# Optimization experiments

Hardware: AMD Instinct MI355X
Metric: run time of the kernel (lower is better)

Reference implementation:

```python
import jax, jax.numpy as jnp
import numpy as np

B, P, N, C, H, E, HORIZON = 4, 8, 10000, 64, 256, 160000, 4


def setup_inputs() -> dict:
    key = jax.random.key(0)
    ks = jax.random.split(key, 32)
    rn = lambda k, shape, s=0.05: jax.random.normal(k, shape, jnp.float32) * s
    inp = {
        "x_seq": rn(ks[0], (B, P, N, C), 1.0),
        "ei0": jax.random.randint(ks[1], (2, E), 0, N, dtype=jnp.int32),
        "ei1": jax.random.randint(ks[2], (2, E), 0, N, dtype=jnp.int32),
        "Wl0": rn(ks[3], (C, H)), "bl0": jnp.zeros((H,), jnp.float32), "Wr0": rn(ks[4], (C, H)),
        "Wl1": rn(ks[5], (C, H)), "bl1": jnp.zeros((H,), jnp.float32), "Wr1": rn(ks[6], (C, H)),
        "Wp": rn(ks[7], (C, H)), "bp": jnp.zeros((C,), jnp.float32),
    }
    i = 8
    for g in ("g1", "g2", "g3"):
        inp[g + "_Wih"] = rn(ks[i], (3 * H, H)); i += 1
        inp[g + "_Whh"] = rn(ks[i], (3 * H, H)); i += 1
        inp[g + "_bih"] = jnp.zeros((3 * H,), jnp.float32)
        inp[g + "_bhh"] = jnp.zeros((3 * H,), jnp.float32)
    return inp


def _sage(x, src, dst, Wl, bl, Wr, n_nodes):
    # PyG SAGEConv (mean aggr): lin_l(mean_j x_j) + lin_r(x_i); lin_r has no bias.
    agg = jax.ops.segment_sum(x[src], dst, num_segments=n_nodes)  # [n, C]
    cnt = jax.ops.segment_sum(jnp.ones((src.shape[0],), x.dtype), dst, num_segments=n_nodes)
    agg = agg / jnp.maximum(cnt, 1.0)[:, None]
    return agg @ Wl + bl + x @ Wr


def _gru(x, h, Wih, Whh, bih, bhh):
    gi = x @ Wih.T + bih
    gh = h @ Whh.T + bhh
    ir, iz, inn = jnp.split(gi, 3, axis=1)
    hr, hz, hn = jnp.split(gh, 3, axis=1)
    r = jax.nn.sigmoid(ir + hr)
    z = jax.nn.sigmoid(iz + hz)
    n = jnp.tanh(inn + r * hn)
    return (1.0 - z) * n + z * h


def reference(x_seq, ei0, ei1,
              Wl0, bl0, Wr0, Wl1, bl1, Wr1,
              g1_Wih, g1_Whh, g1_bih, g1_bhh,
              g2_Wih, g2_Whh, g2_bih, g2_bhh,
              g3_Wih, g3_Whh, g3_bih, g3_bhh,
              Wp, bp):
    Bn = B * N
    off = (jnp.arange(B) * N).astype(ei0.dtype)
    batch = lambda ei: (ei[:, None, :] + off[None, :, None]).reshape(2, -1)
    b0, b1 = batch(ei0), batch(ei1)

    def step(xt, h1, h2, h3):
        c = (_sage(xt, b0[0], b0[1], Wl0, bl0, Wr0, Bn)
             + _sage(xt, b1[0], b1[1], Wl1, bl1, Wr1, Bn))  # HeteroConv aggr='sum'
        c = jax.nn.relu(c)  # dropout is identity in eval
        h1 = _gru(c, h1, g1_Wih, g1_Whh, g1_bih, g1_bhh)
        h2 = _gru(h1, h2, g2_Wih, g2_Whh, g2_bih, g2_bhh)
        h3 = _gru(h2, h3, g3_Wih, g3_Whh, g3_bih, g3_bhh)
        return h1, h2, h3

    h0 = jnp.zeros((Bn, H), x_seq.dtype)
    xs = jnp.transpose(x_seq, (1, 0, 2, 3)).reshape(P, Bn, C)

    def enc_body(carry, xt):
        return step(xt, *carry), None

    (h1, h2, h3), _ = jax.lax.scan(enc_body, (h0, h0, h0), xs)

    def dec_body(carry, _):
        h1, h2, h3, xd = carry
        h1, h2, h3 = step(xd, h1, h2, h3)
        y = h3 @ Wp.T + bp  # [Bn, C]
        return (h1, h2, h3, y), y

    x_dec = x_seq[:, -1].reshape(Bn, C)
    _, ys = jax.lax.scan(dec_body, (h1, h2, h3, x_dec), None, length=HORIZON)
    # ys: [HORIZON, Bn, C] -> [B, HORIZON, N, C]
    return jnp.transpose(ys.reshape(HORIZON, B, N, C), (1, 0, 2, 3))
```

## Files before the change

kernel.cpp:

```cpp
#include <hip/hip_runtime.h>
#include <hip/hip_bf16.h>
#include <cstdint>

#define B_   4
#define P_   8
#define N_   10000
#define C_   64
#define H_   256
#define E_   160000
#define HOR_ 4
#define BN_  (B_ * N_)
#define MPAD 40064

typedef __bf16 bf16;
typedef __attribute__((ext_vector_type(8))) __bf16 bf16x8;
typedef __attribute__((ext_vector_type(4))) float f32x4;

__device__ __forceinline__ void gl2lds16(const bf16* g, bf16* l) {
    __builtin_amdgcn_global_load_lds(
        (const __attribute__((address_space(1))) void*)g,
        (__attribute__((address_space(3))) void*)l, 16, 0, 0);
}

template <int BIAS, int RELU, int OUTBF, int PROJ>
__global__ __launch_bounds__(256) void gemm_k(
    const bf16* __restrict__ A, const bf16* __restrict__ Bt,
    void* __restrict__ Cp, const float* __restrict__ bias,
    int K, int Nn, int tstep)
{
    __shared__ __align__(16) bf16 As[128 * 32];
    __shared__ __align__(16) bf16 Bs[128 * 32];

    const int tid  = threadIdx.x;
    const int m0   = blockIdx.y * 128;
    const int n0   = blockIdx.x * 128;
    const int wave = tid >> 6;
    const int lane = tid & 63;
    const int wm   = (wave >> 1) << 6;
    const int wn   = (wave & 1) << 6;
    const int lr   = lane & 15;
    const int kg   = lane >> 4;

    f32x4 acc[4][4] = {};

    const int r0 = tid >> 2;
    const int k0 = (tid & 3) << 3;

    for (int kk = 0; kk < K; kk += 32) {
        const bf16* ga = A  + (size_t)(m0 + r0) * K + kk + k0;
        const bf16* gb = Bt + (size_t)(n0 + r0) * K + kk + k0;
        gl2lds16(ga,                  As + tid * 8);
        gl2lds16(ga + 64 * (size_t)K, As + 2048 + tid * 8);
        gl2lds16(gb,                  Bs + tid * 8);
        gl2lds16(gb + 64 * (size_t)K, Bs + 2048 + tid * 8);
        __syncthreads();

        bf16x8 af[4], bfv[4];
#pragma unroll
        for (int i = 0; i < 4; ++i)
            af[i] = *reinterpret_cast<const bf16x8*>(&As[(wm + i * 16 + lr) * 32 + kg * 8]);
#pragma unroll
        for (int j = 0; j < 4; ++j)
            bfv[j] = *reinterpret_cast<const bf16x8*>(&Bs[(wn + j * 16 + lr) * 32 + kg * 8]);
#pragma unroll
        for (int i = 0; i < 4; ++i)
#pragma unroll
            for (int j = 0; j < 4; ++j)
                acc[i][j] = __builtin_amdgcn_mfma_f32_16x16x32_bf16(af[i], bfv[j], acc[i][j], 0, 0, 0);
        __syncthreads();
    }

#pragma unroll
    for (int i = 0; i < 4; ++i) {
#pragma unroll
        for (int j = 0; j < 4; ++j) {
#pragma unroll
            for (int v = 0; v < 4; ++v) {
                int row = m0 + wm + i * 16 + kg * 4 + v;
                int col = n0 + wn + j * 16 + lr;
                float val = acc[i][j][v];
                if (BIAS) val += bias[col];
                if (RELU) val = fmaxf(val, 0.f);
                if (PROJ) {
                    if (col < C_ && row < BN_) {
                        int b = row / N_, n = row - b * N_;
                        reinterpret_cast<float*>(Cp)[(((size_t)b * HOR_ + tstep) * N_ + n) * C_ + col] = val;
                    }
                } else if (OUTBF) {
                    reinterpret_cast<bf16*>(Cp)[(size_t)row * Nn + col] = (bf16)val;
                } else {
                    reinterpret_cast<float*>(Cp)[(size_t)row * Nn + col] = val;
                }
            }
        }
    }
}

__global__ __launch_bounds__(256, 2) void gru_fused_k(
    const bf16* __restrict__ X, const bf16* __restrict__ Hc,
    bf16* __restrict__ Hn,
    const bf16* __restrict__ Wih, const bf16* __restrict__ Whh,
    const float* __restrict__ bih, const float* __restrict__ bhh)
{
    const int id    = blockIdx.x;
    const int sblk  = id >> 6;
    const int jblk  = (id >> 3) & 7;
    const int slow  = id & 7;
    const int strip = (sblk << 3) | slow;
    if (strip >= 313) return;

    __shared__ __align__(16) bf16 Xs[128 * 32];
    __shared__ __align__(16) bf16 Hs[128 * 32];
    __shared__ __align__(16) bf16 Ws[6 * 32 * 32];

    const int tid  = threadIdx.x;
    const int m0   = strip * 128;
    const int j0   = jblk * 32;
    const int wave = tid >> 6;
    const int lane = tid & 63;
    const int wm   = (wave >> 1) << 6;
    const int wn   = (wave & 1) << 4;
    const int lr   = lane & 15;
    const int kg   = lane >> 4;

    f32x4 acc[6][4] = {};

    const int r0 = tid >> 2;
    const int k0 = (tid & 3) << 3;

    int wgate[3], wrow[3], wk[3];
#pragma unroll
    for (int c = 0; c < 3; ++c) {
        int f = c * 2048 + tid * 8;
        wgate[c] = f >> 10;
        wrow[c]  = (f >> 5) & 31;
        wk[c]    = f & 31;
    }

    for (int kk = 0; kk < 256; kk += 32) {
        gl2lds16(X  + (size_t)(m0 + r0) * 256 + kk + k0,      Xs + tid * 8);
        gl2lds16(X  + (size_t)(m0 + r0 + 64) * 256 + kk + k0, Xs + 2048 + tid * 8);
        gl2lds16(Hc + (size_t)(m0 + r0) * 256 + kk + k0,      Hs + tid * 8);
        gl2lds16(Hc + (size_t)(m0 + r0 + 64) * 256 + kk + k0, Hs + 2048 + tid * 8);
#pragma unroll
        for (int c = 0; c < 3; ++c) {
            int g = wgate[c];
            const bf16* src = (g < 3)
                ? Wih + (size_t)(g * 256 + j0 + wrow[c]) * 256 + kk + wk[c]
                : Whh + (size_t)((g - 3) * 256 + j0 + wrow[c]) * 256 + kk + wk[c];
            gl2lds16(src, Ws + c * 2048 + tid * 8);
        }
        __syncthreads();

        bf16x8 af[4], ah[4], bw[6];
#pragma unroll
        for (int i = 0; i < 4; ++i) {
            af[i] = *reinterpret_cast<const bf16x8*>(&Xs[(wm + i * 16 + lr) * 32 + kg * 8]);
            ah[i] = *reinterpret_cast<const bf16x8*>(&Hs[(wm + i * 16 + lr) * 32 + kg * 8]);
        }
#pragma unroll
        for (int g = 0; g < 6; ++g)
            bw[g] = *reinterpret_cast<const bf16x8*>(&Ws[g * 1024 + (wn + lr) * 32 + kg * 8]);
#pragma unroll
        for (int g = 0; g < 3; ++g)
#pragma unroll
            for (int i = 0; i < 4; ++i)
                acc[g][i] = __builtin_amdgcn_mfma_f32_16x16x32_bf16(af[i], bw[g], acc[g][i], 0, 0, 0);
#pragma unroll
        for (int g = 3; g < 6; ++g)
#pragma unroll
            for (int i = 0; i < 4; ++i)
                acc[g][i] = __builtin_amdgcn_mfma_f32_16x16x32_bf16(ah[i], bw[g], acc[g][i], 0, 0, 0);
        __syncthreads();
    }

    const int col = j0 + wn + lr;
    const float bi_r = bih[col], bi_z = bih[256 + col], bi_n = bih[512 + col];
    const float bh_r = bhh[col], bh_z = bhh[256 + col], bh_n = bhh[512 + col];
#pragma unroll
    for (int i = 0; i < 4; ++i) {
#pragma unroll
        for (int v = 0; v < 4; ++v) {
            int row = m0 + wm + i * 16 + kg * 4 + v;
            float ir  = acc[0][i][v] + bi_r;
            float iz  = acc[1][i][v] + bi_z;
            float in_ = acc[2][i][v] + bi_n;
            float hr  = acc[3][i][v] + bh_r;
            float hz  = acc[4][i][v] + bh_z;
            float hn  = acc[5][i][v] + bh_n;
            float r = __fdividef(1.f, 1.f + __expf(-(ir + hr)));
            float z = __fdividef(1.f, 1.f + __expf(-(iz + hz)));
            float a = in_ + r * hn;
            a = fminf(fmaxf(a, -15.f), 15.f);
            float t2 = __expf(2.f * a);
            float nn = __fdividef(t2 - 1.f, t2 + 1.f);
            float hold = (float)Hc[(size_t)row * 256 + col];
            Hn[(size_t)row * 256 + col] = (bf16)((1.f - z) * nn + z * hold);
        }
    }
}

struct __attribute__((aligned(8))) bf4 { bf16 b[4]; };

__global__ __launch_bounds__(256) void gather_conv_k(
    const float* __restrict__ xbase, long long sB, long long sN,
    const int* __restrict__ rp0, const int* __restrict__ col0,
    const int* __restrict__ rp1, const int* __restrict__ col1,
    bf16* __restrict__ Aconv)
{
    int wid  = (blockIdx.x * 256 + threadIdx.x) >> 6;
    int lane = threadIdx.x & 63;
    if (wid >= BN_) return;
    int b = wid / N_;
    int n = wid - b * N_;
    int eg = lane >> 4;
    int cl = lane & 15;
    const float* xb = xbase + (size_t)b * sB;

    float4 xv = *reinterpret_cast<const float4*>(&xb[(size_t)n * sN + cl * 4]);

    float4 s0 = {0.f, 0.f, 0.f, 0.f};
    int st = rp0[n], en = rp0[n + 1];
    float d0 = fmaxf((float)(en - st), 1.f);
    for (int e = st + eg; e < en; e += 4) {
        const float4 v = *reinterpret_cast<const float4*>(&xb[(size_t)col0[e] * sN + cl * 4]);
        s0.x += v.x; s0.y += v.y; s0.z += v.z; s0.w += v.w;
    }

    float4 s1 = {0.f, 0.f, 0.f, 0.f};
    st = rp1[n]; en = rp1[n + 1];
    float d1 = fmaxf((float)(en - st), 1.f);
    for (int e = st + eg; e < en; e += 4) {
        const float4 v = *reinterpret_cast<const float4*>(&xb[(size_t)col1[e] * sN + cl * 4]);
        s1.x += v.x; s1.y += v.y; s1.z += v.z; s1.w += v.w;
    }

#pragma unroll
    for (int m = 16; m <= 32; m <<= 1) {
        s0.x += __shfl_xor(s0.x, m, 64); s0.y += __shfl_xor(s0.y, m, 64);
        s0.z += __shfl_xor(s0.z, m, 64); s0.w += __shfl_xor(s0.w, m, 64);
        s1.x += __shfl_xor(s1.x, m, 64); s1.y += __shfl_xor(s1.y, m, 64);
        s1.z += __shfl_xor(s1.z, m, 64); s1.w += __shfl_xor(s1.w, m, 64);
    }

    if (eg == 0) {
        float r0 = 1.f / d0, r1 = 1.f / d1;
        bf16* row = Aconv + (size_t)wid * 192;
        bf4 o;
        o.b[0] = (bf16)(s0.x * r0); o.b[1] = (bf16)(s0.y * r0);
        o.b[2] = (bf16)(s0.z * r0); o.b[3] = (bf16)(s0.w * r0);
        *reinterpret_cast<bf4*>(&row[cl * 4]) = o;
        o.b[0] = (bf16)xv.x; o.b[1] = (bf16)xv.y; o.b[2] = (bf16)xv.z; o.b[3] = (bf16)xv.w;
        *reinterpret_cast<bf4*>(&row[64 + cl * 4]) = o;
        o.b[0] = (bf16)(s1.x * r1); o.b[1] = (bf16)(s1.y * r1);
        o.b[2] = (bf16)(s1.z * r1); o.b[3] = (bf16)(s1.w * r1);
        *reinterpret_cast<bf4*>(&row[128 + cl * 4]) = o;
    }
}

__global__ void count_k(const int* __restrict__ ei, int* __restrict__ cnt) {
    int e = blockIdx.x * 256 + threadIdx.x;
    if (e < E_) atomicAdd(&cnt[ei[E_ + e]], 1);
}

__global__ __launch_bounds__(1024) void scan_k(
    const int* __restrict__ cnt, int* __restrict__ rp, int* __restrict__ fill)
{
    __shared__ int sums[1024];
    int t = threadIdx.x;
    const int chunk = 10;
    int lo = t * chunk;
    int hi = lo + chunk; if (hi > N_) hi = N_;
    int s = 0;
    for (int i = lo; i < hi; ++i) s += cnt[i];
    sums[t] = s;
    __syncthreads();
    for (int off = 1; off < 1024; off <<= 1) {
        int u = (t >= off) ? sums[t - off] : 0;
        __syncthreads();
        sums[t] += u;
        __syncthreads();
    }
    int base = (t == 0) ? 0 : sums[t - 1];
    for (int i = lo; i < hi; ++i) { rp[i] = base; fill[i] = base; base += cnt[i]; }
    if (t == 1023) rp[N_] = sums[1023];
}

__global__ void fill_k(const int* __restrict__ ei, int* __restrict__ fill,
                       int* __restrict__ colarr) {
    int e = blockIdx.x * 256 + threadIdx.x;
    if (e < E_) {
        int p = atomicAdd(&fill[ei[E_ + e]], 1);
        colarr[p] = ei[e];
    }
}

__global__ void cvt_bf16_k(const float* __restrict__ s, bf16* __restrict__ d, int n) {
    int i = blockIdx.x * 256 + threadIdx.x;
    if (i < n) d[i] = (bf16)s[i];
}

__global__ void build_conv_bt_k(const float* __restrict__ Wl0, const float* __restrict__ Wr0,
                                const float* __restrict__ Wl1, const float* __restrict__ Wr1,
                                bf16* __restrict__ Bt) {
    int idx = blockIdx.x * 256 + threadIdx.x;
    if (idx >= 256 * 192) return;
    int n = idx / 192, k = idx - n * 192;
    float v;
    if (k < 64)       v = Wl0[k * 256 + n];
    else if (k < 128) v = Wr0[(k - 64) * 256 + n] + Wr1[(k - 64) * 256 + n];
    else              v = Wl1[(k - 128) * 256 + n];
    Bt[idx] = (bf16)v;
}

__global__ void build_conv_bias_k(const float* __restrict__ bl0, const float* __restrict__ bl1,
                                  float* __restrict__ bias) {
    int i = threadIdx.x;
    if (i < 256) bias[i] = bl0[i] + bl1[i];
}

__global__ void build_proj_k(const float* __restrict__ Wp, const float* __restrict__ bp,
                             bf16* __restrict__ Bt, float* __restrict__ bias) {
    int idx = blockIdx.x * 256 + threadIdx.x;
    if (idx < 128 * 256) {
        int n = idx >> 8, k = idx & 255;
        Bt[idx] = (bf16)(n < 64 ? Wp[n * 256 + k] : 0.f);
    }
    if (idx < 128) bias[idx] = (idx < 64) ? bp[idx] : 0.f;
}

extern "C" void kernel_launch(void* const* d_in, const int* in_sizes, int n_in,
                              void* d_out, int out_size, void* d_ws, size_t ws_size,
                              hipStream_t stream)
{
    const float* x_seq = (const float*)d_in[0];
    const int*   ei0   = (const int*)d_in[1];
    const int*   ei1   = (const int*)d_in[2];
    const float* Wl0   = (const float*)d_in[3];
    const float* bl0   = (const float*)d_in[4];
    const float* Wr0   = (const float*)d_in[5];
    const float* Wl1   = (const float*)d_in[6];
    const float* bl1   = (const float*)d_in[7];
    const float* Wr1   = (const float*)d_in[8];
    const float* Wp    = (const float*)d_in[9];
    const float* bp    = (const float*)d_in[10];
    const float* gWih[3], *gWhh[3], *gbih[3], *gbhh[3];
    for (int g = 0; g < 3; ++g) {
        gWih[g] = (const float*)d_in[11 + 4 * g];
        gWhh[g] = (const float*)d_in[12 + 4 * g];
        gbih[g] = (const float*)d_in[13 + 4 * g];
        gbhh[g] = (const float*)d_in[14 + 4 * g];
    }

    char* p = (char*)d_ws;
    auto alloc = [&](size_t bytes) -> char* {
        char* r = p; p += (bytes + 255) & ~(size_t)255; return r;
    };
    bf16*  Aconv  = (bf16*)alloc((size_t)MPAD * 192 * 2);
    bf16*  cbuf   = (bf16*)alloc((size_t)MPAD * 256 * 2);
    bf16*  hbuf[6];
    for (int g = 0; g < 6; ++g) hbuf[g] = (bf16*)alloc((size_t)MPAD * 256 * 2);
    bf16*  wih[3], *whh[3];
    for (int g = 0; g < 3; ++g) {
        wih[g] = (bf16*)alloc((size_t)768 * 256 * 2);
        whh[g] = (bf16*)alloc((size_t)768 * 256 * 2);
    }
    bf16*  btconv = (bf16*)alloc((size_t)256 * 192 * 2);
    float* bconv  = (float*)alloc(256 * 4);
    bf16*  btproj = (bf16*)alloc((size_t)128 * 256 * 2);
    float* bproj  = (float*)alloc(128 * 4);
    int* cnt0  = (int*)alloc(N_ * 4);
    int* cnt1  = (int*)alloc(N_ * 4);
    int* rp0   = (int*)alloc((N_ + 1) * 4);
    int* rp1   = (int*)alloc((N_ + 1) * 4);
    int* fill0 = (int*)alloc((N_ + 1) * 4);
    int* fill1 = (int*)alloc((N_ + 1) * 4);
    int* col0  = (int*)alloc(E_ * 4);
    int* col1  = (int*)alloc(E_ * 4);

    hipMemsetAsync(Aconv, 0, (size_t)MPAD * 192 * 2, stream);
    for (int g = 0; g < 3; ++g)
        hipMemsetAsync(hbuf[g], 0, (size_t)MPAD * 256 * 2, stream);
    hipMemsetAsync(cnt0, 0, N_ * 4, stream);
    hipMemsetAsync(cnt1, 0, N_ * 4, stream);

    for (int g = 0; g < 3; ++g) {
        cvt_bf16_k<<<768, 256, 0, stream>>>(gWih[g], wih[g], 768 * 256);
        cvt_bf16_k<<<768, 256, 0, stream>>>(gWhh[g], whh[g], 768 * 256);
    }
    build_conv_bt_k<<<192, 256, 0, stream>>>(Wl0, Wr0, Wl1, Wr1, btconv);
    build_conv_bias_k<<<1, 256, 0, stream>>>(bl0, bl1, bconv);
    build_proj_k<<<128, 256, 0, stream>>>(Wp, bp, btproj, bproj);

    count_k<<<(E_ + 255) / 256, 256, 0, stream>>>(ei0, cnt0);
    count_k<<<(E_ + 255) / 256, 256, 0, stream>>>(ei1, cnt1);
    scan_k<<<1, 1024, 0, stream>>>(cnt0, rp0, fill0);
    scan_k<<<1, 1024, 0, stream>>>(cnt1, rp1, fill1);
    fill_k<<<(E_ + 255) / 256, 256, 0, stream>>>(ei0, fill0, col0);
    fill_k<<<(E_ + 255) / 256, 256, 0, stream>>>(ei1, fill1, col1);

    bf16 *hc[3] = { hbuf[0], hbuf[1], hbuf[2] };
    bf16 *hn[3] = { hbuf[3], hbuf[4], hbuf[5] };

    auto do_conv = [&](const float* xb, long long sB, long long sN) {
        gather_conv_k<<<10000, 256, 0, stream>>>(xb, sB, sN, rp0, col0, rp1, col1, Aconv);
        gemm_k<1, 1, 1, 0><<<dim3(2, 313, 1), 256, 0, stream>>>(
            Aconv, btconv, cbuf, bconv, 192, 256, 0);
    };
    auto do_grus = [&]() {
        gru_fused_k<<<2560, 256, 0, stream>>>(
            cbuf, hc[0], hn[0], wih[0], whh[0], gbih[0], gbhh[0]);
        gru_fused_k<<<2560, 256, 0, stream>>>(
            hn[0], hc[1], hn[1], wih[1], whh[1], gbih[1], gbhh[1]);
        gru_fused_k<<<2560, 256, 0, stream>>>(
            hn[1], hc[2], hn[2], wih[2], whh[2], gbih[2], gbhh[2]);
        for (int g = 0; g < 3; ++g) { bf16* t = hc[g]; hc[g] = hn[g]; hn[g] = t; }
    };

    for (int ps = 0; ps < P_; ++ps) {
        do_conv(x_seq + (size_t)ps * N_ * C_, (long long)P_ * N_ * C_, C_);
        do_grus();
    }

    float* out = (float*)d_out;
    for (int t = 0; t < HOR_; ++t) {
        if (t > 0)
            do_conv(out + (size_t)(t - 1) * N_ * C_, (long long)HOR_ * N_ * C_, C_);
        do_grus();
        gemm_k<1, 0, 0, 1><<<dim3(1, 313, 1), 256, 0, stream>>>(
            hc[2], btproj, out, bproj, 256, 128, t);
    }
}
```

Before: 2.782 ms.

## Double-buffer LDS tiles in GEMM and fused GRU kernels to overlap loads

Both the generic GEMM kernel and the fused GRU kernel now keep two LDS buffers per operand. The next K-slice is issued via global_load_lds while MFMAs run on the current slice, and only one barrier is taken per iteration. The aim is to hide global memory latency behind compute. It doubles LDS use per block, which may reduce occupancy, most likely in the GRU kernel, which already declares launch bounds of 2 blocks per CU.

```diff
diff --git a/kernel.cpp b/kernel.cpp
--- a/kernel.cpp
+++ b/kernel.cpp
@@ -28,8 +28,8 @@
     void* __restrict__ Cp, const float* __restrict__ bias,
     int K, int Nn, int tstep)
 {
-    __shared__ __align__(16) bf16 As[128 * 32];
-    __shared__ __align__(16) bf16 Bs[128 * 32];
+    __shared__ __align__(16) bf16 As[2][128 * 32];
+    __shared__ __align__(16) bf16 Bs[2][128 * 32];
 
     const int tid  = threadIdx.x;
     const int m0   = blockIdx.y * 128;
@@ -46,29 +46,40 @@
     const int r0 = tid >> 2;
     const int k0 = (tid & 3) << 3;
 
-    for (int kk = 0; kk < K; kk += 32) {
+    auto stage = [&](int buf, int kk) {
         const bf16* ga = A  + (size_t)(m0 + r0) * K + kk + k0;
         const bf16* gb = Bt + (size_t)(n0 + r0) * K + kk + k0;
-        gl2lds16(ga,                  As + tid * 8);
-        gl2lds16(ga + 64 * (size_t)K, As + 2048 + tid * 8);
-        gl2lds16(gb,                  Bs + tid * 8);
-        gl2lds16(gb + 64 * (size_t)K, Bs + 2048 + tid * 8);
-        __syncthreads();
-
+        gl2lds16(ga,                  &As[buf][tid * 8]);
+        gl2lds16(ga + 64 * (size_t)K, &As[buf][2048 + tid * 8]);
+        gl2lds16(gb,                  &Bs[buf][tid * 8]);
+        gl2lds16(gb + 64 * (size_t)K, &Bs[buf][2048 + tid * 8]);
+    };
+
+    auto compute = [&](int cb) {
         bf16x8 af[4], bfv[4];
 #pragma unroll
         for (int i = 0; i < 4; ++i)
-            af[i] = *reinterpret_cast<const bf16x8*>(&As[(wm + i * 16 + lr) * 32 + kg * 8]);
+            af[i] = *reinterpret_cast<const bf16x8*>(&As[cb][(wm + i * 16 + lr) * 32 + kg * 8]);
 #pragma unroll
         for (int j = 0; j < 4; ++j)
-            bfv[j] = *reinterpret_cast<const bf16x8*>(&Bs[(wn + j * 16 + lr) * 32 + kg * 8]);
+            bfv[j] = *reinterpret_cast<const bf16x8*>(&Bs[cb][(wn + j * 16 + lr) * 32 + kg * 8]);
 #pragma unroll
         for (int i = 0; i < 4; ++i)
 #pragma unroll
             for (int j = 0; j < 4; ++j)
                 acc[i][j] = __builtin_amdgcn_mfma_f32_16x16x32_bf16(af[i], bfv[j], acc[i][j], 0, 0, 0);
+    };
+
+    stage(0, 0);
+    __syncthreads();
+    int cur = 0;
+    for (int kk = 32; kk < K; kk += 32) {
+        stage(cur ^ 1, kk);
+        compute(cur);
         __syncthreads();
-    }
+        cur ^= 1;
+    }
+    compute(cur);
 
 #pragma unroll
     for (int i = 0; i < 4; ++i) {
@@ -109,9 +120,9 @@
     const int strip = (sblk << 3) | slow;
     if (strip >= 313) return;
 
-    __shared__ __align__(16) bf16 Xs[128 * 32];
-    __shared__ __align__(16) bf16 Hs[128 * 32];
-    __shared__ __align__(16) bf16 Ws[6 * 32 * 32];
+    __shared__ __align__(16) bf16 Xs[2][128 * 32];
+    __shared__ __align__(16) bf16 Hs[2][128 * 32];
+    __shared__ __align__(16) bf16 Ws[2][6 * 32 * 32];
 
     const int tid  = threadIdx.x;
     const int m0   = strip * 128;
@@ -137,30 +148,31 @@
         wk[c]    = f & 31;
     }
 
-    for (int kk = 0; kk < 256; kk += 32) {
-        gl2lds16(X  + (size_t)(m0 + r0) * 256 + kk + k0,      Xs + tid * 8);
-        gl2lds16(X  + (size_t)(m0 + r0 + 64) * 256 + kk + k0, Xs + 2048 + tid * 8);
-        gl2lds16(Hc + (size_t)(m0 + r0) * 256 + kk + k0,      Hs + tid * 8);
-        gl2lds16(Hc + (size_t)(m0 + r0 + 64) * 256 + kk + k0, Hs + 2048 + tid * 8);
+    auto stage = [&](int buf, int kk) {
+        gl2lds16(X  + (size_t)(m0 + r0) * 256 + kk + k0,      &Xs[buf][tid * 8]);
+        gl2lds16(X  + (size_t)(m0 + r0 + 64) * 256 + kk + k0, &Xs[buf][2048 + tid * 8]);
+        gl2lds16(Hc + (size_t)(m0 + r0) * 256 + kk + k0,      &Hs[buf][tid * 8]);
+        gl2lds16(Hc + (size_t)(m0 + r0 + 64) * 256 + kk + k0, &Hs[buf][2048 + tid * 8]);
 #pragma unroll
         for (int c = 0; c < 3; ++c) {
             int g = wgate[c];
             const bf16* src = (g < 3)
                 ? Wih + (size_t)(g * 256 + j0 + wrow[c]) * 256 + kk + wk[c]
                 : Whh + (size_t)((g - 3) * 256 + j0 + wrow[c]) * 256 + kk + wk[c];
-            gl2lds16(src, Ws + c * 2048 + tid * 8);
+            gl2lds16(src, &Ws[buf][c * 2048 + tid * 8]);
         }
-        __syncthreads();
-
+    };
+
+    auto compute = [&](int cb) {
         bf16x8 af[4], ah[4], bw[6];
 #pragma unroll
         for (int i = 0; i < 4; ++i) {
-            af[i] = *reinterpret_cast<const bf16x8*>(&Xs[(wm + i * 16 + lr) * 32 + kg * 8]);
-            ah[i] = *reinterpret_cast<const bf16x8*>(&Hs[(wm + i * 16 + lr) * 32 + kg * 8]);
+            af[i] = *reinterpret_cast<const bf16x8*>(&Xs[cb][(wm + i * 16 + lr) * 32 + kg * 8]);
+            ah[i] = *reinterpret_cast<const bf16x8*>(&Hs[cb][(wm + i * 16 + lr) * 32 + kg * 8]);
         }
 #pragma unroll
         for (int g = 0; g < 6; ++g)
-            bw[g] = *reinterpret_cast<const bf16x8*>(&Ws[g * 1024 + (wn + lr) * 32 + kg * 8]);
+            bw[g] = *reinterpret_cast<const bf16x8*>(&Ws[cb][g * 1024 + (wn + lr) * 32 + kg * 8]);
 #pragma unroll
         for (int g = 0; g < 3; ++g)
 #pragma unroll
@@ -171,8 +183,18 @@
 #pragma unroll
             for (int i = 0; i < 4; ++i)
                 acc[g][i] = __builtin_amdgcn_mfma_f32_16x16x32_bf16(ah[i], bw[g], acc[g][i], 0, 0, 0);
+    };
+
+    stage(0, 0);
+    __syncthreads();
+    int cur = 0;
+    for (int kk = 32; kk < 256; kk += 32) {
+        stage(cur ^ 1, kk);
+        compute(cur);
         __syncthreads();
-    }
+        cur ^= 1;
+    }
+    compute(cur);
 
     const int col = j0 + wn + lr;
     const float bi_r = bih[col], bi_z = bih[256 + col], bi_n = bih[512 + col];
```

Measured after the change: 3.080 ms. 10.7% more time.
